# Performance work log

Hardware: AMD Instinct MI355X
Metric: run time of the kernel (lower is better)

The kernel has to match this reference:

```python
import jax, jax.numpy as jnp
import numpy as np

N = 50000      # nodes
E = 1000000    # directed edges
G = 1000       # graphs (molecules) in the batch
D_NODE = 133
D_EDGE = 147
D_H = 128
D_OUT = 1


def _lrelu(v):
    # torch.nn.functional.leaky_relu default negative_slope = 0.01
    return jnp.where(v >= 0, v, 0.01 * v)


def setup_inputs() -> dict:
    key = jax.random.key(0)
    ks = jax.random.split(key, 10)
    s = 0.05
    return {
        "x": jax.random.normal(ks[0], (N, D_NODE), jnp.float32),
        "concat_feats": jax.random.normal(ks[1], (E, D_EDGE), jnp.float32),
        "srt_concat_batch": jax.random.randint(ks[2], (E,), 0, N),
        "end_concat_batch": jax.random.randint(ks[3], (E,), 0, N),
        "num_concat_feats": E,
        "batch": jnp.sort(jax.random.randint(ks[4], (N,), 0, G)),
        "W_init": s * jax.random.normal(ks[5], (D_H, D_EDGE), jnp.float32),
        "b_init": jnp.zeros((D_H,), jnp.float32),
        "W_h1": s * jax.random.normal(ks[6], (D_H, D_H), jnp.float32),
        "b_h1": jnp.zeros((D_H,), jnp.float32),
        "W_mol": s * jax.random.normal(ks[7], (D_H, D_H), jnp.float32),
        "b_mol": jnp.zeros((D_H,), jnp.float32),
        "W_out": s * jax.random.normal(ks[8], (D_OUT, D_H), jnp.float32),
        "b_out": jnp.zeros((D_OUT,), jnp.float32),
    }


def reference(x, concat_feats, srt_concat_batch, end_concat_batch,
              num_concat_feats, batch,
              W_init, b_init, W_h1, b_h1, W_mol, b_mol, W_out, b_out):
    n = x.shape[0]

    def mp(h):
        # scatter_add over end nodes, gather at srt nodes, subtract reverse contribution
        agg = jax.ops.segment_sum(h, end_concat_batch, num_segments=n)
        return agg[srt_concat_batch] - h[end_concat_batch]

    h0 = _lrelu(concat_feats @ W_init.T + b_init)                 # [E, D_H]
    h1 = _lrelu(h0 + mp(h0) @ W_h1.T + b_h1)
    h2 = _lrelu(h1 + mp(h1) @ W_h1.T + b_h1)
    h3 = _lrelu(h2 + mp(h2) @ W_h1.T + b_h1)

    h_node = jax.ops.segment_sum(h3, srt_concat_batch, num_segments=n)  # [N, D_H]
    atom_embs = _lrelu(h_node @ W_mol.T + b_mol)
    # F.normalize(p=2, dim=1) with eps=1e-12
    norms = jnp.maximum(jnp.linalg.norm(atom_embs, axis=1, keepdims=True), 1e-12)
    hg = jax.ops.segment_sum(atom_embs / norms, batch, num_segments=G)  # [G, D_H]
    out = hg @ W_out.T + b_out                                          # [G, D_OUT]
    return (out, atom_embs)
```

## Files before the change

### kernel.cpp

```cpp
#include <hip/hip_runtime.h>

#define NN 50000
#define NE 1000000
#define NG 1000
#define KE 147
#define DH 128

using u16 = unsigned short;
typedef __attribute__((ext_vector_type(8))) short bf16x8;
typedef __attribute__((ext_vector_type(4))) float f32x4;

__device__ __forceinline__ float lrelu(float v){ return fmaxf(v, 0.01f*v); }
__device__ __forceinline__ float bf2f(u16 u){ unsigned int x = ((unsigned int)u)<<16; float f; __builtin_memcpy(&f,&x,4); return f; }
__device__ __forceinline__ u16 f2bf(float f){ unsigned int x; __builtin_memcpy(&x,&f,4); x += 0x7fffu + ((x>>16)&1u); return (u16)(x>>16); }

__global__ __launch_bounds__(256) void hist_kernel(const int* __restrict__ endi, const int* __restrict__ srt,
                                                   int* __restrict__ cntE, int* __restrict__ cntS){
  for (int i = blockIdx.x*256 + threadIdx.x; i < NE; i += gridDim.x*256){
    atomicAdd(&cntE[endi[i]], 1);
    atomicAdd(&cntS[srt[i]], 1);
  }
}

__global__ __launch_bounds__(1024) void scan2_kernel(const int* __restrict__ cntE, int* __restrict__ offE,
                                                     const int* __restrict__ cntS, int* __restrict__ offS){
  const int* deg = blockIdx.x ? cntS : cntE;
  int* off = blockIdx.x ? offS : offE;
  __shared__ int wsum[17];
  const int t = threadIdx.x, lane = t & 63, wv = t >> 6;
  int carry = 0;
  for (int base = 0; base < 50176; base += 1024){
    const int i = base + t;
    int v = (i < NN) ? deg[i] : 0;
    int s = v;
    #pragma unroll
    for (int d = 1; d < 64; d <<= 1){
      int x = __shfl_up(s, d);
      if (lane >= d) s += x;
    }
    if (lane == 63) wsum[wv] = s;
    __syncthreads();
    if (t == 0){
      int run = 0;
      #pragma unroll
      for (int k = 0; k < 16; ++k){ int x = wsum[k]; wsum[k] = run; run += x; }
      wsum[16] = run;
    }
    __syncthreads();
    if (i <= NN) off[i] = carry + wsum[wv] + s - v;
    carry += wsum[16];
    __syncthreads();
  }
}

__global__ __launch_bounds__(256) void scatter_kernel(const int* __restrict__ endi, const int* __restrict__ srt,
                                                      int* __restrict__ curE, int* __restrict__ curS,
                                                      int* __restrict__ rankE, int* __restrict__ srtE,
                                                      int* __restrict__ listS, int* __restrict__ endS){
  for (int i = blockIdx.x*256 + threadIdx.x; i < NE; i += gridDim.x*256){
    const int e = endi[i], s = srt[i];
    int p = atomicAdd(&curE[e], 1);
    rankE[i] = p; srtE[p] = s;
    int q = atomicAdd(&curS[s], 1);
    listS[q] = i; endS[q] = e;
  }
}

__global__ __launch_bounds__(256) void post_kernel(const int* __restrict__ listS, const int* __restrict__ rankE,
                                                   int* __restrict__ listS2){
  for (int i = blockIdx.x*256 + threadIdx.x; i < NE; i += gridDim.x*256)
    listS2[i] = rankE[listS[i]];
}

__global__ __launch_bounds__(256) void convertW_kernel(const float* __restrict__ W1, const float* __restrict__ W0,
                                                       u16* __restrict__ Wbf1, u16* __restrict__ Wbf0){
  int i = blockIdx.x*256 + threadIdx.x;
  if (i < 128*128) Wbf1[i] = f2bf(W1[i]);
  if (i < 128*160){
    int j = i/160, k = i - j*160;
    Wbf0[i] = (k < KE) ? f2bf(W0[j*KE + k]) : (u16)0;
  }
}

__global__ __launch_bounds__(256) void layer0_mfma(const float* __restrict__ cf, const u16* __restrict__ Wbf0,
                                                   const float* __restrict__ b, const int* __restrict__ rankE,
                                                   u16* __restrict__ h){
  __shared__ __align__(16) u16 As[128*168];
  const int t = threadIdx.x, lane = t & 63, wv = t >> 6;
  const int wr = wv >> 1, wc = wv & 1;
  const long e0 = (long)blockIdx.x * 128;

  bf16x8 bfrag[5][4];
  const int jb = lane & 15, kg8 = (lane >> 4)*8;
  #pragma unroll
  for (int fc = 0; fc < 4; ++fc)
    #pragma unroll
    for (int ks = 0; ks < 5; ++ks)
      bfrag[ks][fc] = *(const bf16x8*)&Wbf0[(size_t)(wc*64 + fc*16 + jb)*160 + ks*32 + kg8];

  const long gbase = e0 * KE;
  if (e0 + 128 <= NE){
    for (int i = t; i < 128*KE; i += 256){
      int r = i / KE, c = i - r*KE;
      As[r*168 + c] = f2bf(cf[gbase + i]);
    }
  } else {
    for (int i = t; i < 128*168; i += 256) As[i] = 0;
    __syncthreads();
    for (int i = t; i < 128*KE; i += 256){
      long g = gbase + i;
      if (g < (long)NE*KE){ int r = i / KE, c = i - r*KE; As[r*168 + c] = f2bf(cf[g]); }
    }
  }
  for (int i = t; i < 128*13; i += 256){
    int r = i / 13, c = i - r*13;
    As[r*168 + 147 + c] = 0;
  }
  __syncthreads();

  f32x4 acc[4][4];
  #pragma unroll
  for (int fr = 0; fr < 4; ++fr)
    #pragma unroll
    for (int fc = 0; fc < 4; ++fc){ acc[fr][fc][0]=0.f; acc[fr][fc][1]=0.f; acc[fr][fc][2]=0.f; acc[fr][fc][3]=0.f; }
  const int ar = lane & 15;
  #pragma unroll
  for (int ks = 0; ks < 5; ++ks){
    bf16x8 a[4];
    #pragma unroll
    for (int fr = 0; fr < 4; ++fr)
      a[fr] = *(const bf16x8*)&As[(wr*64 + fr*16 + ar)*168 + ks*32 + kg8];
    #pragma unroll
    for (int fr = 0; fr < 4; ++fr)
      #pragma unroll
      for (int fc = 0; fc < 4; ++fc)
        acc[fr][fc] = __builtin_amdgcn_mfma_f32_16x16x32_bf16(a[fr], bfrag[ks][fc], acc[fr][fc], 0, 0, 0);
  }

  float* Clds = (float*)As;
  const int cr0 = (lane >> 4)*4, cc = lane & 15;
  for (int half = 0; half < 2; ++half){
    __syncthreads();
    if (wr == half){
      #pragma unroll
      for (int fr = 0; fr < 4; ++fr)
        #pragma unroll
        for (int fc = 0; fc < 4; ++fc)
          #pragma unroll
          for (int r = 0; r < 4; ++r)
            Clds[(fr*16 + cr0 + r)*132 + wc*64 + fc*16 + cc] = acc[fr][fc][r];
    }
    __syncthreads();
    const int rr = t & 63, cw = t >> 6;
    const long e = e0 + half*64 + rr;
    if (e < NE){
      const int orow = rankE[e];
      u16* hp = &h[(size_t)orow*DH + cw*32];
      #pragma unroll
      for (int c8 = 0; c8 < 4; ++c8){
        float4 c0v = *(const float4*)&Clds[rr*132 + cw*32 + c8*8];
        float4 c1v = *(const float4*)&Clds[rr*132 + cw*32 + c8*8 + 4];
        float4 b0 = *(const float4*)&b[cw*32 + c8*8];
        float4 b1 = *(const float4*)&b[cw*32 + c8*8 + 4];
        ushort4 n0, n1;
        n0.x = f2bf(lrelu(c0v.x + b0.x)); n0.y = f2bf(lrelu(c0v.y + b0.y));
        n0.z = f2bf(lrelu(c0v.z + b0.z)); n0.w = f2bf(lrelu(c0v.w + b0.w));
        n1.x = f2bf(lrelu(c1v.x + b1.x)); n1.y = f2bf(lrelu(c1v.y + b1.y));
        n1.z = f2bf(lrelu(c1v.z + b1.z)); n1.w = f2bf(lrelu(c1v.w + b1.w));
        *(ushort4*)&hp[c8*8] = n0; *(ushort4*)&hp[c8*8+4] = n1;
      }
    }
  }
}

__global__ __launch_bounds__(256) void aggE_kernel(const u16* __restrict__ h, const int* __restrict__ off,
                                                   float* __restrict__ agg){
  const int t = threadIdx.x, lane = t & 63, wv = t >> 6;
  const int n = blockIdx.x*4 + wv;
  if (n >= NN) return;
  const int lo = off[n], hi = off[n+1];
  const int c4 = (lane & 31)*4, sub = lane >> 5;
  float a0=0.f, a1=0.f, a2=0.f, a3=0.f;
  for (int i = lo + sub; i < hi; i += 2){
    ushort4 hv = *(const ushort4*)&h[(size_t)i*DH + c4];
    a0 += bf2f(hv.x); a1 += bf2f(hv.y); a2 += bf2f(hv.z); a3 += bf2f(hv.w);
  }
  a0 += __shfl_xor(a0, 32); a1 += __shfl_xor(a1, 32);
  a2 += __shfl_xor(a2, 32); a3 += __shfl_xor(a3, 32);
  if (sub == 0) *(float4*)&agg[(size_t)n*DH + c4] = make_float4(a0,a1,a2,a3);
}

__global__ __launch_bounds__(256) void pq_gemm(const float* __restrict__ agg, const u16* __restrict__ h,
                                               const int* __restrict__ rankE, const u16* __restrict__ Wbf,
                                               const float* __restrict__ b, float* __restrict__ P,
                                               float* __restrict__ Q){
  __shared__ u16 Alds[128][136];
  const int t = threadIdx.x, lane = t & 63, wv = t >> 6;
  const int wr = wv >> 1, wc = wv & 1;
  const int r0 = blockIdx.x * 128;

  bf16x8 bfrag[4][4];
  const int jb = lane & 15, kg8 = (lane >> 4)*8;
  #pragma unroll
  for (int fc = 0; fc < 4; ++fc)
    #pragma unroll
    for (int ks = 0; ks < 4; ++ks)
      bfrag[ks][fc] = *(const bf16x8*)&Wbf[(size_t)(wc*64 + fc*16 + jb)*128 + ks*32 + kg8];

  {
    const int rt = t >> 1, half = t & 1;
    const int gr = r0 + rt;
    u16* dst = &Alds[rt][half*64];
    if (gr < NN){
      const float4* src = (const float4*)&agg[(size_t)gr*DH + half*64];
      #pragma unroll
      for (int q = 0; q < 16; ++q){
        float4 x = src[q];
        ushort4 o; o.x=f2bf(x.x); o.y=f2bf(x.y); o.z=f2bf(x.z); o.w=f2bf(x.w);
        *(ushort4*)&dst[q*4] = o;
      }
    } else if (gr < 2*NN){
      const int row = rankE[gr - NN];
      const ushort4* src = (const ushort4*)&h[(size_t)row*DH + half*64];
      #pragma unroll
      for (int q = 0; q < 16; ++q) *(ushort4*)&dst[q*4] = src[q];
    } else {
      ushort4 z; z.x=0; z.y=0; z.z=0; z.w=0;
      #pragma unroll
      for (int q = 0; q < 16; ++q) *(ushort4*)&dst[q*4] = z;
    }
  }
  __syncthreads();

  f32x4 acc[4][4];
  #pragma unroll
  for (int fr = 0; fr < 4; ++fr)
    #pragma unroll
    for (int fc = 0; fc < 4; ++fc){ acc[fr][fc][0]=0.f; acc[fr][fc][1]=0.f; acc[fr][fc][2]=0.f; acc[fr][fc][3]=0.f; }
  const int ar = lane & 15;
  #pragma unroll
  for (int ks = 0; ks < 4; ++ks){
    bf16x8 a[4];
    #pragma unroll
    for (int fr = 0; fr < 4; ++fr)
      a[fr] = *(const bf16x8*)&Alds[wr*64 + fr*16 + ar][ks*32 + kg8];
    #pragma unroll
    for (int fr = 0; fr < 4; ++fr)
      #pragma unroll
      for (int fc = 0; fc < 4; ++fc)
        acc[fr][fc] = __builtin_amdgcn_mfma_f32_16x16x32_bf16(a[fr], bfrag[ks][fc], acc[fr][fc], 0, 0, 0);
  }

  const int crow = (lane >> 4)*4, ccol = lane & 15;
  #pragma unroll
  for (int fr = 0; fr < 4; ++fr){
    #pragma unroll
    for (int r = 0; r < 4; ++r){
      const int grow = r0 + wr*64 + fr*16 + crow + r;
      if (grow < NN){
        #pragma unroll
        for (int fc = 0; fc < 4; ++fc){
          const int col = wc*64 + fc*16 + ccol;
          P[(size_t)grow*DH + col] = acc[fr][fc][r] + b[col];
        }
      } else if (grow < 2*NN){
        #pragma unroll
        for (int fc = 0; fc < 4; ++fc){
          const int col = wc*64 + fc*16 + ccol;
          Q[(size_t)(grow-NN)*DH + col] = acc[fr][fc][r];
        }
      }
    }
  }
}

__global__ __launch_bounds__(256) void fused_mid(u16* __restrict__ h, const float* __restrict__ P,
                                                 const float* __restrict__ Q, const int* __restrict__ srtE,
                                                 const int* __restrict__ off, float* __restrict__ agg){
  const int t = threadIdx.x, lane = t & 63, wv = t >> 6;
  const int n = blockIdx.x*4 + wv;
  if (n >= NN) return;
  const int lo = off[n], hi = off[n+1];
  const int c4 = (lane & 31)*4, sub = lane >> 5;
  const float4 qv = *(const float4*)&Q[(size_t)n*DH + c4];
  float a0=0.f, a1=0.f, a2=0.f, a3=0.f;
  for (int i = lo + sub; i < hi; i += 2){
    const int s = srtE[i];
    ushort4 hv = *(const ushort4*)&h[(size_t)i*DH + c4];
    float4 pv = *(const float4*)&P[(size_t)s*DH + c4];
    float v0 = lrelu(bf2f(hv.x) + pv.x - qv.x);
    float v1 = lrelu(bf2f(hv.y) + pv.y - qv.y);
    float v2 = lrelu(bf2f(hv.z) + pv.z - qv.z);
    float v3 = lrelu(bf2f(hv.w) + pv.w - qv.w);
    ushort4 o; o.x=f2bf(v0); o.y=f2bf(v1); o.z=f2bf(v2); o.w=f2bf(v3);
    *(ushort4*)&h[(size_t)i*DH + c4] = o;
    a0 += v0; a1 += v1; a2 += v2; a3 += v3;
  }
  a0 += __shfl_xor(a0, 32); a1 += __shfl_xor(a1, 32);
  a2 += __shfl_xor(a2, 32); a3 += __shfl_xor(a3, 32);
  if (sub == 0) *(float4*)&agg[(size_t)n*DH + c4] = make_float4(a0,a1,a2,a3);
}

__global__ __launch_bounds__(256) void fused_last(const u16* __restrict__ h, const float* __restrict__ P,
                                                  const float* __restrict__ Q, const int* __restrict__ endS,
                                                  const int* __restrict__ listS2, const int* __restrict__ off,
                                                  float* __restrict__ hnode){
  const int t = threadIdx.x, lane = t & 63, wv = t >> 6;
  const int s = blockIdx.x*4 + wv;
  if (s >= NN) return;
  const int lo = off[s], hi = off[s+1];
  const int c4 = (lane & 31)*4, sub = lane >> 5;
  const float4 pv = *(const float4*)&P[(size_t)s*DH + c4];
  float a0=0.f, a1=0.f, a2=0.f, a3=0.f;
  for (int i = lo + sub; i < hi; i += 2){
    const int row = listS2[i];
    const int d = endS[i];
    ushort4 hv = *(const ushort4*)&h[(size_t)row*DH + c4];
    float4 qv = *(const float4*)&Q[(size_t)d*DH + c4];
    a0 += lrelu(bf2f(hv.x) + pv.x - qv.x);
    a1 += lrelu(bf2f(hv.y) + pv.y - qv.y);
    a2 += lrelu(bf2f(hv.z) + pv.z - qv.z);
    a3 += lrelu(bf2f(hv.w) + pv.w - qv.w);
  }
  a0 += __shfl_xor(a0, 32); a1 += __shfl_xor(a1, 32);
  a2 += __shfl_xor(a2, 32); a3 += __shfl_xor(a3, 32);
  if (sub == 0) *(float4*)&hnode[(size_t)s*DH + c4] = make_float4(a0,a1,a2,a3);
}

__global__ __launch_bounds__(256) void node_kernel(
    const float* __restrict__ hn, const float* __restrict__ W,
    const float* __restrict__ b, float* __restrict__ atom, float* __restrict__ normed)
{
  __shared__ float Wt[64*132];
  __shared__ float ms[32*DH];
  const int t = threadIdx.x;
  const int r0 = blockIdx.x * 32;
  const int jg = t & 31, eg = t >> 5;
  for (int idx = t; idx < 32*DH; idx += 256) {
    const int r = r0 + (idx >> 7);
    ms[idx] = (r < NN) ? hn[(size_t)r*DH + (idx & 127)] : 0.f;
  }
  float acc[4][4] = {};
  for (int c = 0; c < 2; ++c) {
    __syncthreads();
    for (int idx = t; idx < 128*64; idx += 256) {
      const int j = idx >> 6, kl = idx & 63;
      Wt[kl*132 + j] = W[j*DH + c*64 + kl];
    }
    __syncthreads();
    #pragma unroll 4
    for (int kl = 0; kl < 64; ++kl) {
      const float4 w = *(const float4*)&Wt[kl*132 + jg*4];
      const int kg = c*64 + kl;
      #pragma unroll
      for (int i = 0; i < 4; ++i) {
        const float mv = ms[(eg*4+i)*DH + kg];
        acc[i][0] += mv*w.x; acc[i][1] += mv*w.y; acc[i][2] += mv*w.z; acc[i][3] += mv*w.w;
      }
    }
  }
  float bj[4];
  #pragma unroll
  for (int c2 = 0; c2 < 4; ++c2) bj[c2] = b[jg*4 + c2];
  #pragma unroll
  for (int i = 0; i < 4; ++i) {
    const int r = r0 + eg*4 + i;
    float v[4]; float ss = 0.f;
    #pragma unroll
    for (int c2 = 0; c2 < 4; ++c2) { v[c2] = lrelu(acc[i][c2] + bj[c2]); ss += v[c2]*v[c2]; }
    ss += __shfl_xor(ss, 1); ss += __shfl_xor(ss, 2); ss += __shfl_xor(ss, 4);
    ss += __shfl_xor(ss, 8); ss += __shfl_xor(ss, 16);
    if (r < NN) {
      *(float4*)&atom[(size_t)r*DH + jg*4] = make_float4(v[0],v[1],v[2],v[3]);
      const float inv = 1.f / fmaxf(sqrtf(ss), 1e-12f);
      *(float4*)&normed[(size_t)r*DH + jg*4] = make_float4(v[0]*inv,v[1]*inv,v[2]*inv,v[3]*inv);
    }
  }
}

__global__ __launch_bounds__(128) void graph_out_kernel(const float* __restrict__ normed, const int* __restrict__ batch,
                                                        const float* __restrict__ Wo, const float* __restrict__ bo,
                                                        float* __restrict__ out){
  const int g = blockIdx.x, t = threadIdx.x;
  int lo, hi;
  { int a=0, bb=NN; while(a<bb){ int m=(a+bb)>>1; if (batch[m] < g) a=m+1; else bb=m; } lo=a; }
  { int a=lo, bb=NN; while(a<bb){ int m=(a+bb)>>1; if (batch[m] < g+1) a=m+1; else bb=m; } hi=a; }
  float s = 0.f;
  for (int n = lo; n < hi; ++n) s += normed[(size_t)n*DH + t];
  float v = s * Wo[t];
  #pragma unroll
  for (int d2 = 1; d2 < 64; d2 <<= 1) v += __shfl_xor(v, d2);
  __shared__ float red[2];
  if ((t & 63) == 0) red[t >> 6] = v;
  __syncthreads();
  if (t == 0) out[g] = red[0] + red[1] + bo[0];
}

extern "C" void kernel_launch(void* const* d_in, const int* in_sizes, int n_in,
                              void* d_out, int out_size, void* d_ws, size_t ws_size,
                              hipStream_t stream)
{
  const float* cf     = (const float*)d_in[1];
  const int*   srt    = (const int*)d_in[2];
  const int*   endi   = (const int*)d_in[3];
  const int*   batch  = (const int*)d_in[5];
  const float* W_init = (const float*)d_in[6];
  const float* b_init = (const float*)d_in[7];
  const float* W_h1   = (const float*)d_in[8];
  const float* b_h1   = (const float*)d_in[9];
  const float* W_mol  = (const float*)d_in[10];
  const float* b_mol  = (const float*)d_in[11];
  const float* W_out  = (const float*)d_in[12];
  const float* b_out  = (const float*)d_in[13];

  float* out  = (float*)d_out;
  float* atom = out + NG;

  char* ws = (char*)d_ws;
  u16*   h      = (u16*)(ws);
  float* agg    = (float*)(ws + 256000000);
  float* P      = (float*)(ws + 281600000);
  float* Q      = (float*)(ws + 307200000);
  int*   srtE   = (int*)(ws + 332800000);
  int*   listS  = (int*)(ws + 336800000);
  int*   endS   = (int*)(ws + 340800000);
  int*   rankE  = (int*)(ws + 344800000);
  int*   listS2 = (int*)(ws + 348800000);
  int*   offE   = (int*)(ws + 352800000);
  int*   offS   = (int*)(ws + 353000704);
  int*   curE   = (int*)(ws + 353201408);
  int*   curS   = (int*)(ws + 353402112);
  u16*   Wbf1   = (u16*)(ws + 353602816);
  u16*   Wbf0   = (u16*)(ws + 353635584);
  float* hnode  = agg;
  float* normed = (float*)(ws);

  hipMemsetAsync(curE, 0, 200704, stream);
  hipMemsetAsync(curS, 0, 200704, stream);
  hist_kernel<<<1024, 256, 0, stream>>>(endi, srt, curE, curS);
  scan2_kernel<<<2, 1024, 0, stream>>>(curE, offE, curS, offS);
  hipMemcpyAsync(curE, offE, (size_t)NN*4, hipMemcpyDeviceToDevice, stream);
  hipMemcpyAsync(curS, offS, (size_t)NN*4, hipMemcpyDeviceToDevice, stream);
  scatter_kernel<<<1024, 256, 0, stream>>>(endi, srt, curE, curS, rankE, srtE, listS, endS);
  post_kernel<<<1024, 256, 0, stream>>>(listS, rankE, listS2);
  convertW_kernel<<<80, 256, 0, stream>>>(W_h1, W_init, Wbf1, Wbf0);

  layer0_mfma<<<(NE + 127)/128, 256, 0, stream>>>(cf, Wbf0, b_init, rankE, h);
  aggE_kernel<<<NN/4, 256, 0, stream>>>(h, offE, agg);

  for (int l = 0; l < 2; ++l){
    pq_gemm<<<(2*NN + 127)/128, 256, 0, stream>>>(agg, h, rankE, Wbf1, b_h1, P, Q);
    fused_mid<<<NN/4, 256, 0, stream>>>(h, P, Q, srtE, offE, agg);
  }
  pq_gemm<<<(2*NN + 127)/128, 256, 0, stream>>>(agg, h, rankE, Wbf1, b_h1, P, Q);
  fused_last<<<NN/4, 256, 0, stream>>>(h, P, Q, endS, listS2, offS, hnode);

  node_kernel<<<(NN + 31)/32, 256, 0, stream>>>(hnode, W_mol, b_mol, atom, normed);
  graph_out_kernel<<<NG, 128, 0, stream>>>(normed, batch, W_out, b_out, out);
}
```

Measured before the change: 1.291 ms.

## Permute hidden-channel layout so MFMA outputs store directly without LDS staging

Stores hidden features in a permuted channel order (cpi) so each lane's MFMA accumulator columns are contiguous, letting layer0 and pq_gemm write float4/ushort4 directly from registers instead of staging through LDS. The permutation is folded into W_h1 columns, the biases and W_mol's input columns so results stay consistent. Layer0 also drops the LDS tile for the edge features and loads A fragments straight from global memory with per-element bf16 conversion, removing barriers and shared-memory traffic. The direct strided global loads of fp32 rows may coalesce worse than the previous cooperative tile load.

```diff
diff --git a/kernel.cpp b/kernel.cpp
--- a/kernel.cpp
+++ b/kernel.cpp
@@ -13,6 +13,7 @@
 __device__ __forceinline__ float lrelu(float v){ return fmaxf(v, 0.01f*v); }
 __device__ __forceinline__ float bf2f(u16 u){ unsigned int x = ((unsigned int)u)<<16; float f; __builtin_memcpy(&f,&x,4); return f; }
 __device__ __forceinline__ u16 f2bf(float f){ unsigned int x; __builtin_memcpy(&x,&f,4); x += 0x7fffu + ((x>>16)&1u); return (u16)(x>>16); }
+__device__ __host__ __forceinline__ int cpi(int p){ return (p & 64) | ((p & 3) << 4) | ((p & 63) >> 2); }
 
 __global__ __launch_bounds__(256) void hist_kernel(const int* __restrict__ endi, const int* __restrict__ srt,
                                                    int* __restrict__ cntE, int* __restrict__ cntS){
@@ -73,63 +74,59 @@
 }
 
 __global__ __launch_bounds__(256) void convertW_kernel(const float* __restrict__ W1, const float* __restrict__ W0,
-                                                       u16* __restrict__ Wbf1, u16* __restrict__ Wbf0){
+                                                       const float* __restrict__ b0, const float* __restrict__ b1,
+                                                       u16* __restrict__ Wb1, u16* __restrict__ Wb0,
+                                                       float* __restrict__ bp0, float* __restrict__ bp1){
   int i = blockIdx.x*256 + threadIdx.x;
-  if (i < 128*128) Wbf1[i] = f2bf(W1[i]);
+  if (i < 128*128){
+    int j = i >> 7, k = i & 127;
+    Wb1[i] = f2bf(W1[j*DH + cpi(k)]);
+  }
   if (i < 128*160){
     int j = i/160, k = i - j*160;
-    Wbf0[i] = (k < KE) ? f2bf(W0[j*KE + k]) : (u16)0;
-  }
-}
-
-__global__ __launch_bounds__(256) void layer0_mfma(const float* __restrict__ cf, const u16* __restrict__ Wbf0,
-                                                   const float* __restrict__ b, const int* __restrict__ rankE,
+    Wb0[i] = (k < KE) ? f2bf(W0[j*KE + k]) : (u16)0;
+  }
+  if (i < 128){ bp0[i] = b0[cpi(i)]; bp1[i] = b1[cpi(i)]; }
+}
+
+__global__ __launch_bounds__(256) void layer0_mfma(const float* __restrict__ cf, const u16* __restrict__ Wb0,
+                                                   const float* __restrict__ bp0, const int* __restrict__ rankE,
                                                    u16* __restrict__ h){
-  __shared__ __align__(16) u16 As[128*168];
   const int t = threadIdx.x, lane = t & 63, wv = t >> 6;
   const int wr = wv >> 1, wc = wv & 1;
   const long e0 = (long)blockIdx.x * 128;
+  const int q = lane & 15, kg8 = (lane >> 4) * 8;
 
   bf16x8 bfrag[5][4];
-  const int jb = lane & 15, kg8 = (lane >> 4)*8;
   #pragma unroll
   for (int fc = 0; fc < 4; ++fc)
     #pragma unroll
     for (int ks = 0; ks < 5; ++ks)
-      bfrag[ks][fc] = *(const bf16x8*)&Wbf0[(size_t)(wc*64 + fc*16 + jb)*160 + ks*32 + kg8];
-
-  const long gbase = e0 * KE;
-  if (e0 + 128 <= NE){
-    for (int i = t; i < 128*KE; i += 256){
-      int r = i / KE, c = i - r*KE;
-      As[r*168 + c] = f2bf(cf[gbase + i]);
-    }
-  } else {
-    for (int i = t; i < 128*168; i += 256) As[i] = 0;
-    __syncthreads();
-    for (int i = t; i < 128*KE; i += 256){
-      long g = gbase + i;
-      if (g < (long)NE*KE){ int r = i / KE, c = i - r*KE; As[r*168 + c] = f2bf(cf[g]); }
-    }
-  }
-  for (int i = t; i < 128*13; i += 256){
-    int r = i / 13, c = i - r*13;
-    As[r*168 + 147 + c] = 0;
-  }
-  __syncthreads();
+      bfrag[ks][fc] = *(const bf16x8*)&Wb0[(size_t)(wc*64 + fc*16 + q)*160 + ks*32 + kg8];
 
   f32x4 acc[4][4];
   #pragma unroll
   for (int fr = 0; fr < 4; ++fr)
     #pragma unroll
     for (int fc = 0; fc < 4; ++fc){ acc[fr][fc][0]=0.f; acc[fr][fc][1]=0.f; acc[fr][fc][2]=0.f; acc[fr][fc][3]=0.f; }
-  const int ar = lane & 15;
+
   #pragma unroll
   for (int ks = 0; ks < 5; ++ks){
     bf16x8 a[4];
     #pragma unroll
-    for (int fr = 0; fr < 4; ++fr)
-      a[fr] = *(const bf16x8*)&As[(wr*64 + fr*16 + ar)*168 + ks*32 + kg8];
+    for (int fr = 0; fr < 4; ++fr){
+      const long e = e0 + wr*64 + fr*16 + q;
+      const float* rp = cf + (size_t)e*KE;
+      bf16x8 av;
+      #pragma unroll
+      for (int j = 0; j < 8; ++j){
+        const int kk = ks*32 + kg8 + j;
+        float v = 0.f;
+        if (e < (long)NE && (ks < 4 || kk < KE)) v = rp[kk];
+        av[j] = (short)f2bf(v);
+      }
+      a[fr] = av;
+    }
     #pragma unroll
     for (int fr = 0; fr < 4; ++fr)
       #pragma unroll
@@ -137,37 +134,20 @@
         acc[fr][fc] = __builtin_amdgcn_mfma_f32_16x16x32_bf16(a[fr], bfrag[ks][fc], acc[fr][fc], 0, 0, 0);
   }
 
-  float* Clds = (float*)As;
-  const int cr0 = (lane >> 4)*4, cc = lane & 15;
-  for (int half = 0; half < 2; ++half){
-    __syncthreads();
-    if (wr == half){
-      #pragma unroll
-      for (int fr = 0; fr < 4; ++fr)
-        #pragma unroll
-        for (int fc = 0; fc < 4; ++fc)
-          #pragma unroll
-          for (int r = 0; r < 4; ++r)
-            Clds[(fr*16 + cr0 + r)*132 + wc*64 + fc*16 + cc] = acc[fr][fc][r];
-    }
-    __syncthreads();
-    const int rr = t & 63, cw = t >> 6;
-    const long e = e0 + half*64 + rr;
-    if (e < NE){
-      const int orow = rankE[e];
-      u16* hp = &h[(size_t)orow*DH + cw*32];
-      #pragma unroll
-      for (int c8 = 0; c8 < 4; ++c8){
-        float4 c0v = *(const float4*)&Clds[rr*132 + cw*32 + c8*8];
-        float4 c1v = *(const float4*)&Clds[rr*132 + cw*32 + c8*8 + 4];
-        float4 b0 = *(const float4*)&b[cw*32 + c8*8];
-        float4 b1 = *(const float4*)&b[cw*32 + c8*8 + 4];
-        ushort4 n0, n1;
-        n0.x = f2bf(lrelu(c0v.x + b0.x)); n0.y = f2bf(lrelu(c0v.y + b0.y));
-        n0.z = f2bf(lrelu(c0v.z + b0.z)); n0.w = f2bf(lrelu(c0v.w + b0.w));
-        n1.x = f2bf(lrelu(c1v.x + b1.x)); n1.y = f2bf(lrelu(c1v.y + b1.y));
-        n1.z = f2bf(lrelu(c1v.z + b1.z)); n1.w = f2bf(lrelu(c1v.w + b1.w));
-        *(ushort4*)&hp[c8*8] = n0; *(ushort4*)&hp[c8*8+4] = n1;
+  const float4 bb = *(const float4*)&bp0[wc*64 + q*4];
+  #pragma unroll
+  for (int fr = 0; fr < 4; ++fr){
+    #pragma unroll
+    for (int r = 0; r < 4; ++r){
+      const long ee = e0 + wr*64 + fr*16 + (lane>>4)*4 + r;
+      if (ee < (long)NE){
+        const int row = rankE[ee];
+        ushort4 o;
+        o.x = f2bf(lrelu(acc[fr][0][r] + bb.x));
+        o.y = f2bf(lrelu(acc[fr][1][r] + bb.y));
+        o.z = f2bf(lrelu(acc[fr][2][r] + bb.z));
+        o.w = f2bf(lrelu(acc[fr][3][r] + bb.w));
+        *(ushort4*)&h[(size_t)row*DH + wc*64 + q*4] = o;
       }
     }
   }
@@ -191,21 +171,21 @@
 }
 
 __global__ __launch_bounds__(256) void pq_gemm(const float* __restrict__ agg, const u16* __restrict__ h,
-                                               const int* __restrict__ rankE, const u16* __restrict__ Wbf,
-                                               const float* __restrict__ b, float* __restrict__ P,
+                                               const int* __restrict__ rankE, const u16* __restrict__ Wb1,
+                                               const float* __restrict__ bp1, float* __restrict__ P,
                                                float* __restrict__ Q){
   __shared__ u16 Alds[128][136];
   const int t = threadIdx.x, lane = t & 63, wv = t >> 6;
   const int wr = wv >> 1, wc = wv & 1;
   const int r0 = blockIdx.x * 128;
+  const int q = lane & 15, kg8 = (lane >> 4)*8;
 
   bf16x8 bfrag[4][4];
-  const int jb = lane & 15, kg8 = (lane >> 4)*8;
   #pragma unroll
   for (int fc = 0; fc < 4; ++fc)
     #pragma unroll
     for (int ks = 0; ks < 4; ++ks)
-      bfrag[ks][fc] = *(const bf16x8*)&Wbf[(size_t)(wc*64 + fc*16 + jb)*128 + ks*32 + kg8];
+      bfrag[ks][fc] = *(const bf16x8*)&Wb1[(size_t)(wc*64 + fc*16 + q)*128 + ks*32 + kg8];
 
   {
     const int rt = t >> 1, half = t & 1;
@@ -214,20 +194,20 @@
     if (gr < NN){
       const float4* src = (const float4*)&agg[(size_t)gr*DH + half*64];
       #pragma unroll
-      for (int q = 0; q < 16; ++q){
-        float4 x = src[q];
+      for (int p = 0; p < 16; ++p){
+        float4 x = src[p];
         ushort4 o; o.x=f2bf(x.x); o.y=f2bf(x.y); o.z=f2bf(x.z); o.w=f2bf(x.w);
-        *(ushort4*)&dst[q*4] = o;
+        *(ushort4*)&dst[p*4] = o;
       }
     } else if (gr < 2*NN){
       const int row = rankE[gr - NN];
       const ushort4* src = (const ushort4*)&h[(size_t)row*DH + half*64];
       #pragma unroll
-      for (int q = 0; q < 16; ++q) *(ushort4*)&dst[q*4] = src[q];
+      for (int p = 0; p < 16; ++p) *(ushort4*)&dst[p*4] = src[p];
     } else {
       ushort4 z; z.x=0; z.y=0; z.z=0; z.w=0;
       #pragma unroll
-      for (int q = 0; q < 16; ++q) *(ushort4*)&dst[q*4] = z;
+      for (int p = 0; p < 16; ++p) *(ushort4*)&dst[p*4] = z;
     }
   }
   __syncthreads();
@@ -237,13 +217,12 @@
   for (int fr = 0; fr < 4; ++fr)
     #pragma unroll
     for (int fc = 0; fc < 4; ++fc){ acc[fr][fc][0]=0.f; acc[fr][fc][1]=0.f; acc[fr][fc][2]=0.f; acc[fr][fc][3]=0.f; }
-  const int ar = lane & 15;
   #pragma unroll
   for (int ks = 0; ks < 4; ++ks){
     bf16x8 a[4];
     #pragma unroll
     for (int fr = 0; fr < 4; ++fr)
-      a[fr] = *(const bf16x8*)&Alds[wr*64 + fr*16 + ar][ks*32 + kg8];
+      a[fr] = *(const bf16x8*)&Alds[wr*64 + fr*16 + q][ks*32 + kg8];
     #pragma unroll
     for (int fr = 0; fr < 4; ++fr)
       #pragma unroll
@@ -251,24 +230,19 @@
         acc[fr][fc] = __builtin_amdgcn_mfma_f32_16x16x32_bf16(a[fr], bfrag[ks][fc], acc[fr][fc], 0, 0, 0);
   }
 
-  const int crow = (lane >> 4)*4, ccol = lane & 15;
+  const float4 bb = *(const float4*)&bp1[wc*64 + q*4];
   #pragma unroll
   for (int fr = 0; fr < 4; ++fr){
     #pragma unroll
     for (int r = 0; r < 4; ++r){
-      const int grow = r0 + wr*64 + fr*16 + crow + r;
+      const int grow = r0 + wr*64 + fr*16 + (lane>>4)*4 + r;
       if (grow < NN){
-        #pragma unroll
-        for (int fc = 0; fc < 4; ++fc){
-          const int col = wc*64 + fc*16 + ccol;
-          P[(size_t)grow*DH + col] = acc[fr][fc][r] + b[col];
-        }
+        float4 val = make_float4(acc[fr][0][r] + bb.x, acc[fr][1][r] + bb.y,
+                                 acc[fr][2][r] + bb.z, acc[fr][3][r] + bb.w);
+        *(float4*)&P[(size_t)grow*DH + wc*64 + q*4] = val;
       } else if (grow < 2*NN){
-        #pragma unroll
-        for (int fc = 0; fc < 4; ++fc){
-          const int col = wc*64 + fc*16 + ccol;
-          Q[(size_t)(grow-NN)*DH + col] = acc[fr][fc][r];
-        }
+        float4 val = make_float4(acc[fr][0][r], acc[fr][1][r], acc[fr][2][r], acc[fr][3][r]);
+        *(float4*)&Q[(size_t)(grow-NN)*DH + wc*64 + q*4] = val;
       }
     }
   }
@@ -345,7 +319,7 @@
     __syncthreads();
     for (int idx = t; idx < 128*64; idx += 256) {
       const int j = idx >> 6, kl = idx & 63;
-      Wt[kl*132 + j] = W[j*DH + c*64 + kl];
+      Wt[kl*132 + j] = W[j*DH + c*64 + ((kl&3)*16 + (kl>>2))];
     }
     __syncthreads();
     #pragma unroll 4
@@ -430,8 +404,10 @@
   int*   offS   = (int*)(ws + 353000704);
   int*   curE   = (int*)(ws + 353201408);
   int*   curS   = (int*)(ws + 353402112);
-  u16*   Wbf1   = (u16*)(ws + 353602816);
-  u16*   Wbf0   = (u16*)(ws + 353635584);
+  u16*   Wb1    = (u16*)(ws + 353602816);
+  u16*   Wb0    = (u16*)(ws + 353635584);
+  float* bp0    = (float*)(ws + 353676544);
+  float* bp1    = (float*)(ws + 353677056);
   float* hnode  = agg;
   float* normed = (float*)(ws);
 
@@ -443,16 +419,16 @@
   hipMemcpyAsync(curS, offS, (size_t)NN*4, hipMemcpyDeviceToDevice, stream);
   scatter_kernel<<<1024, 256, 0, stream>>>(endi, srt, curE, curS, rankE, srtE, listS, endS);
   post_kernel<<<1024, 256, 0, stream>>>(listS, rankE, listS2);
-  convertW_kernel<<<80, 256, 0, stream>>>(W_h1, W_init, Wbf1, Wbf0);
-
-  layer0_mfma<<<(NE + 127)/128, 256, 0, stream>>>(cf, Wbf0, b_init, rankE, h);
+  convertW_kernel<<<80, 256, 0, stream>>>(W_h1, W_init, b_init, b_h1, Wb1, Wb0, bp0, bp1);
+
+  layer0_mfma<<<(NE + 127)/128, 256, 0, stream>>>(cf, Wb0, bp0, rankE, h);
   aggE_kernel<<<NN/4, 256, 0, stream>>>(h, offE, agg);
 
   for (int l = 0; l < 2; ++l){
-    pq_gemm<<<(2*NN + 127)/128, 256, 0, stream>>>(agg, h, rankE, Wbf1, b_h1, P, Q);
+    pq_gemm<<<(2*NN + 127)/128, 256, 0, stream>>>(agg, h, rankE, Wb1, bp1, P, Q);
     fused_mid<<<NN/4, 256, 0, stream>>>(h, P, Q, srtE, offE, agg);
   }
-  pq_gemm<<<(2*NN + 127)/128, 256, 0, stream>>>(agg, h, rankE, Wbf1, b_h1, P, Q);
+  pq_gemm<<<(2*NN + 127)/128, 256, 0, stream>>>(agg, h, rankE, Wb1, bp1, P, Q);
   fused_last<<<NN/4, 256, 0, stream>>>(h, P, Q, endS, listS2, offS, hnode);
 
   node_kernel<<<(NN + 31)/32, 256, 0, stream>>>(hnode, W_mol, b_mol, atom, normed);
```

New measurement: 1.351 ms. +4.6%, slower.
